# Optimization experiments

Hardware: AMD Instinct MI355X
Metric: run time of the kernel (lower is better)

The kernel has to match this reference:

```python
import jax, jax.numpy as jnp
import numpy as np

K = 32        # number of negative samples
MARGIN = 1.0  # ranking margin
N_NODES = 8192
D_FEAT = 128
N_ANCHOR = 512
CHUNK = 128   # anchor chunk for cdist to bound the [chunk,N,d] intermediate


def l1_cdist(X, Y):
    # X: [A, d], Y: [N, d] -> [A, N]; chunk over A so the abs-diff tensor
    # is [CHUNK, N, d] (~0.5GB here) instead of [A, N, d].
    A, d = X.shape
    def f(xc):  # xc: [CHUNK, d]
        return jnp.sum(jnp.abs(xc[:, None, :] - Y[None, :, :]), axis=-1)
    out = jax.lax.map(f, X.reshape(-1, CHUNK, d))  # [A/CHUNK, CHUNK, N]
    return out.reshape(A, Y.shape[0])


def l1_rowdist(a, b):
    # a, b: [..., d] -> [...]: per-row L1 distance
    return jnp.sum(jnp.abs(a - b), axis=-1)


def setup_inputs() -> dict:
    key = jax.random.key(0)
    k1, k2, k3, k4 = jax.random.split(key, 4)
    out1 = jax.random.normal(k1, (N_NODES, D_FEAT), dtype=jnp.float32)
    out2 = jax.random.normal(k2, (N_NODES, D_FEAT), dtype=jnp.float32)
    anchor1 = jax.random.randint(k3, (N_ANCHOR,), 0, N_NODES, dtype=jnp.int64 if jax.config.jax_enable_x64 else jnp.int32)
    anchor2 = jax.random.randint(k4, (N_ANCHOR,), 0, N_NODES, dtype=jnp.int64 if jax.config.jax_enable_x64 else jnp.int32)
    return {"out1": out1, "out2": out2, "anchor1": anchor1, "anchor2": anchor2}


def reference(out1, out2, anchor1, anchor2):
    a1 = out1[anchor1]  # [A, d]
    a2 = out2[anchor2]  # [A, d]

    # Negative sampling: k NEAREST nodes in the other graph (argsort ascending,
    # take first k). Indices only -> no gradient path (matches numpy detach).
    _, neg1 = jax.lax.top_k(-l1_cdist(a1, out2), K)  # [A, K] into out2
    _, neg2 = jax.lax.top_k(-l1_cdist(a2, out1), K)  # [A, K] into out1

    neg_emb1 = out2[neg1]  # [A, K, d]
    neg_emb2 = out1[neg2]  # [A, K, d]

    D = l1_rowdist(a1, a2) + MARGIN          # [A]
    B1 = -l1_rowdist(a1[:, None, :], neg_emb1)  # [A, K]
    B2 = -l1_rowdist(a2[:, None, :], neg_emb2)  # [A, K]

    L1 = jnp.sum(jax.nn.relu(D[:, None] + B1))
    L2 = jnp.sum(jax.nn.relu(D[:, None] + B2))
    return (L1 + L2) / (anchor1.shape[0] * K)
```

## Files before the change

kernel.cpp:

```cpp
#include <hip/hip_runtime.h>


#define NN 8192
#define DF 128
#define NA 512
#define KK 32
#define CCAP 256


__device__ __forceinline__ float wave_reduce_f(float x) {
#pragma unroll
  for (int off = 32; off > 0; off >>= 1) x += __shfl_down(x, off);
  return x;
}

__device__ __forceinline__ int wave_reduce_i(int x) {
#pragma unroll
  for (int off = 32; off > 0; off >>= 1) x += __shfl_down(x, off);
  return x;
}

__device__ __forceinline__ unsigned umin2(unsigned a, unsigned b) {
  return a < b ? a : b;
}

__device__ __forceinline__ unsigned minpair(unsigned w_) {
  return umin2(w_ & 0xFFFFu, w_ >> 16);
}

__device__ __forceinline__ unsigned sad8(unsigned a, unsigned b,
                                         unsigned acc) {
#if __has_builtin(__builtin_amdgcn_sad_u8)
  return __builtin_amdgcn_sad_u8(a, b, acc);
#else
#pragma unroll
  for (int i = 0; i < 4; ++i) {
    const int av = (int)((a >> (8 * i)) & 0xFFu);
    const int bv = (int)((b >> (8 * i)) & 0xFFu);
    acc += (unsigned)(av > bv ? av - bv : bv - av);
  }
  return acc;
#endif
}

__device__ __forceinline__ unsigned q8(float x) {
  const float f = fmaxf(fmaf(x, 16.0f, 128.5f), 0.0f);
  return umin2((unsigned)f, 255u);
}

__device__ __forceinline__ unsigned q8x4(float4 v) {
  return q8(v.x) | (q8(v.y) << 8) | (q8(v.z) << 16) | (q8(v.w) << 24);
}

__device__ __forceinline__ uint2 quant8u8(float4 a, float4 b) {
  uint2 r;
  r.x = q8x4(a);
  r.y = q8x4(b);
  return r;
}


__global__ __launch_bounds__(256, 2) void dist_kernel(
    const float* __restrict__ out1, const float* __restrict__ out2,
    const int* __restrict__ anchor1, const int* __restrict__ anchor2,
    unsigned short* __restrict__ dist16, float* __restrict__ out) {
  const int tid = threadIdx.x;
  const int nb = blockIdx.x;
  const int ab = blockIdx.y;
  const int dir = blockIdx.z;
  const float* nodes = dir ? out1 : out2;
  const float* asrc = dir ? out2 : out1;
  const int* aidx = dir ? anchor2 : anchor1;
  const int n0 = nb * 128;
  const int a0 = ab * 128;

  if (nb == 0 && ab == 0 && dir == 0 && tid == 0) *out = 0.0f;

  __shared__ union {
    struct {
      unsigned nds[128][34];
      unsigned ads[128][34];
    } t;
    unsigned short stage16[32][136];
  } sm;
  __shared__ int aind[128];

  if (tid < 128) aind[tid] = aidx[a0 + tid];

  unsigned acc[8][8];
#pragma unroll
  for (int i = 0; i < 8; ++i)
#pragma unroll
    for (int j = 0; j < 8; ++j) acc[i][j] = 0u;

  const int tn = tid & 15;
  const int ta = tid >> 4;

  __syncthreads();
#pragma unroll
  for (int r = 0; r < 8; ++r) {
    const int f = tid + 256 * r;
    const int row = f >> 4;
    const int q = f & 15;
    const float* src = nodes + (size_t)(n0 + row) * DF + q * 8;
    const float4 v0 = *(const float4*)(src);
    const float4 v1 = *(const float4*)(src + 4);
    *(uint2*)&sm.t.nds[row][q * 2] = quant8u8(v0, v1);
  }
#pragma unroll
  for (int r = 0; r < 8; ++r) {
    const int f = tid + 256 * r;
    const int row = f >> 4;
    const int q = f & 15;
    const float* src = asrc + (size_t)aind[row] * DF + q * 8;
    const float4 v0 = *(const float4*)(src);
    const float4 v1 = *(const float4*)(src + 4);
    *(uint2*)&sm.t.ads[row][q * 2] = quant8u8(v0, v1);
  }
  __syncthreads();

#pragma unroll 1
  for (int d8 = 0; d8 < 16; ++d8) {
    uint2 nv[8], av[8];
#pragma unroll
    for (int i = 0; i < 8; ++i)
      nv[i] = *(const uint2*)&sm.t.nds[tn + 16 * i][d8 * 2];
#pragma unroll
    for (int j = 0; j < 8; ++j)
      av[j] = *(const uint2*)&sm.t.ads[ta + 16 * j][d8 * 2];
#pragma unroll
    for (int i = 0; i < 8; ++i)
#pragma unroll
      for (int j = 0; j < 8; ++j) {
        const unsigned s = sad8(nv[i].x, av[j].x, acc[i][j]);
        acc[i][j] = sad8(nv[i].y, av[j].y, s);
      }
  }

  const size_t rowbase = (size_t)(dir * NA + a0) * NN + n0;
#pragma unroll
  for (int stg = 0; stg < 4; ++stg) {
    __syncthreads();
#pragma unroll
    for (int jn = 0; jn < 2; ++jn) {
      const int jj = stg * 2 + jn;
#pragma unroll
      for (int i = 0; i < 8; ++i) {
        sm.stage16[ta + 16 * jn][tn + 16 * i] =
            (unsigned short)umin2(acc[i][jj], 65535u);
      }
    }
    __syncthreads();
#pragma unroll
    for (int s = 0; s < 2; ++s) {
      const int f = tid + 256 * s;
      const int r = f >> 4;
      const int c8 = f & 15;
      const uint4 v = *(const uint4*)&sm.stage16[r][c8 * 8];
      *(uint4*)(dist16 + rowbase + (size_t)(stg * 32 + r) * NN + c8 * 8) = v;
    }
  }
}


__global__ __launch_bounds__(256) void select_kernel(
    const unsigned short* __restrict__ dist16, const float* __restrict__ out1,
    const float* __restrict__ out2, const int* __restrict__ anchor1,
    const int* __restrict__ anchor2, float* __restrict__ out) {
  const int tid = threadIdx.x;
  const int lane = tid & 63, w = tid >> 6;
  const int row = blockIdx.x;
  const int a = row & (NA - 1);

  __shared__ unsigned mins[256];
  __shared__ unsigned cand[CCAP];
  __shared__ int cnt;
  __shared__ unsigned Tsh;
  __shared__ float dred[2];
  __shared__ int wcnt[4];
  __shared__ float fred[4];
  __shared__ int cred[4];

  const uint4* drow = (const uint4*)(dist16 + (size_t)row * NN);
  const float inv = 1.0f / 16.0f;

  {
    float p = 0.f;
    if (tid < DF) {
      const int r1 = anchor1[a];
      const int r2 = anchor2[a];
      p = fabsf(out1[(size_t)r1 * DF + tid] - out2[(size_t)r2 * DF + tid]);
    }
    p = wave_reduce_f(p);
    if (tid < DF && lane == 0) dred[w] = p;
  }
  if (tid == 0) cnt = 0;

  uint4 v4[4];
#pragma unroll
  for (int g = 0; g < 4; ++g) v4[g] = drow[tid + 256 * g];

  unsigned m = 0xFFFFFFFFu;
#pragma unroll
  for (int g = 0; g < 4; ++g) {
    m = umin2(m, minpair(v4[g].x));
    m = umin2(m, minpair(v4[g].y));
    m = umin2(m, minpair(v4[g].z));
    m = umin2(m, minpair(v4[g].w));
  }
  mins[tid] = m;
  __syncthreads();

  if (w == 0) {
    const unsigned pm =
        umin2(umin2(mins[lane], mins[lane + 64]),
              umin2(mins[lane + 128], mins[lane + 192]));
    unsigned T = 0;
#pragma unroll 1
    for (int b = 15; b >= 0; --b) {
      const unsigned mid = T | (1u << b);
      if ((int)__popcll(__ballot(pm < mid)) < KK) T = mid;
    }
    if (lane == 0) Tsh = T;
  }
  __syncthreads();
  const unsigned T = Tsh;

#pragma unroll
  for (int g = 0; g < 4; ++g) {
    const unsigned ww[4] = {v4[g].x, v4[g].y, v4[g].z, v4[g].w};
#pragma unroll
    for (int k = 0; k < 4; ++k) {
      const unsigned lo = ww[k] & 0xFFFFu, hi = ww[k] >> 16;
      if (lo <= T) { int q = atomicAdd(&cnt, 1); if (q < CCAP) cand[q] = lo; }
      if (hi <= T) { int q = atomicAdd(&cnt, 1); if (q < CCAP) cand[q] = hi; }
    }
  }
  __syncthreads();
  const int C = cnt;
  const float Dv = dred[0] + dred[1] + 1.0f;

  if (C <= CCAP) {
    if (w != 0) return;
    unsigned v[4];
#pragma unroll
    for (int k = 0; k < 4; ++k)
      v[k] = (lane + 64 * k < C) ? cand[lane + 64 * k] : 0xFFFFFFFFu;

    unsigned P = 0;
#pragma unroll 1
    for (int b = 15; b >= 0; --b) {
      const unsigned mid = P | (1u << b);
      int c = 0;
#pragma unroll
      for (int k = 0; k < 4; ++k) c += (int)__popcll(__ballot(v[k] < mid));
      if (c < KK) P = mid;
    }

    float s = 0.f;
    int c = 0;
#pragma unroll
    for (int k = 0; k < 4; ++k) {
      c += (int)__popcll(__ballot(v[k] < P));
      if (v[k] < P) {
        const float t = Dv - (float)v[k] * inv;
        s += (t > 0.f) ? t : 0.f;
      }
    }
    s = wave_reduce_f(s);
    if (lane == 0) {
      float tt = Dv - (float)P * inv;
      if (tt < 0.f) tt = 0.f;
      atomicAdd(out, (s + (float)(KK - c) * tt) * (1.0f / (float)(NA * KK)));
    }
  } else {
    unsigned P = 0;
#pragma unroll 1
    for (int b = 15; b >= 0; --b) {
      const unsigned mid = P | (1u << b);
      int c = 0;
#pragma unroll
      for (int g = 0; g < 4; ++g) {
        const unsigned ww[4] = {v4[g].x, v4[g].y, v4[g].z, v4[g].w};
#pragma unroll
        for (int k = 0; k < 4; ++k) {
          c += (int)__popcll(__ballot((ww[k] & 0xFFFFu) < mid));
          c += (int)__popcll(__ballot((ww[k] >> 16) < mid));
        }
      }
      if (lane == 0) wcnt[w] = c;
      __syncthreads();
      const int tot = wcnt[0] + wcnt[1] + wcnt[2] + wcnt[3];
      __syncthreads();
      if (tot < KK) P = mid;
    }
    float s = 0.f;
    int c = 0;
#pragma unroll
    for (int g = 0; g < 4; ++g) {
      const unsigned ww[4] = {v4[g].x, v4[g].y, v4[g].z, v4[g].w};
#pragma unroll
      for (int k = 0; k < 4; ++k) {
        const unsigned lo = ww[k] & 0xFFFFu, hi = ww[k] >> 16;
        if (lo < P) {
          const float t = Dv - (float)lo * inv;
          s += (t > 0.f) ? t : 0.f;
          c += 1;
        }
        if (hi < P) {
          const float t = Dv - (float)hi * inv;
          s += (t > 0.f) ? t : 0.f;
          c += 1;
        }
      }
    }
    s = wave_reduce_f(s);
    c = wave_reduce_i(c);
    if (lane == 0) {
      fred[w] = s;
      cred[w] = c;
    }
    __syncthreads();
    if (tid == 0) {
      const float stot = fred[0] + fred[1] + fred[2] + fred[3];
      const int ctot = cred[0] + cred[1] + cred[2] + cred[3];
      float tt = Dv - (float)P * inv;
      if (tt < 0.f) tt = 0.f;
      atomicAdd(out,
                (stot + (float)(KK - ctot) * tt) * (1.0f / (float)(NA * KK)));
    }
  }
}


__device__ __forceinline__ float compute_D_block(
    const float* __restrict__ out1, const float* __restrict__ out2,
    const int* __restrict__ anchor1, const int* __restrict__ anchor2, int a) {
  __shared__ float dred[4];
  const int tid = threadIdx.x;
  float p = 0.f;
  if (tid < DF) {
    const int r1 = anchor1[a];
    const int r2 = anchor2[a];
    p = fabsf(out1[(size_t)r1 * DF + tid] - out2[(size_t)r2 * DF + tid]);
  }
  p = wave_reduce_f(p);
  const int lane = tid & 63, wid = tid >> 6;
  if (lane == 0) dred[wid] = p;
  __syncthreads();
  return dred[0] + dred[1] + dred[2] + dred[3] + 1.0f;
}

__global__ __launch_bounds__(256) void fused_kernel(
    const float* __restrict__ out1, const float* __restrict__ out2,
    const int* __restrict__ anchor1, const int* __restrict__ anchor2,
    float* __restrict__ out) {
  const int tid = threadIdx.x;
  const int row = blockIdx.x;
  const int dir = row >> 9;
  const int a = row & (NA - 1);
  const float* nodes = dir ? out1 : out2;
  const float* asrc = dir ? out2 : out1;
  const int* aidx = dir ? anchor2 : anchor1;

  __shared__ float ars[DF];
  __shared__ int redi[4];
  __shared__ float redf[4];
  if (tid < DF / 4) {
    const int arow = aidx[a];
    *(float4*)&ars[tid * 4] =
        *(const float4*)(asrc + (size_t)arow * DF + tid * 4);
  }
  __syncthreads();

  unsigned u[32];
  for (int i = 0; i < 32; ++i) {
    const int n = tid + 256 * i;
    const float4* nrow = (const float4*)(nodes + (size_t)n * DF);
    float dsum = 0.f;
    for (int d4 = 0; d4 < DF / 4; ++d4) {
      const float4 t = nrow[d4];
      const float4 av = *(const float4*)&ars[d4 * 4];
      dsum += fabsf(t.x - av.x) + fabsf(t.y - av.y) + fabsf(t.z - av.z) +
              fabsf(t.w - av.w);
    }
    u[i] = __float_as_uint(dsum);
  }
  __syncthreads();

  const float Dv = compute_D_block(out1, out2, anchor1, anchor2, a);
  const int lane = tid & 63, wid = tid >> 6;

  unsigned P = 0;
#pragma unroll 1
  for (int b = 30; b >= 0; --b) {
    const unsigned mid = P | (1u << b);
    int c = 0;
#pragma unroll
    for (int i = 0; i < 32; ++i) c += (u[i] < mid) ? 1 : 0;
    c = wave_reduce_i(c);
    __syncthreads();
    if (lane == 0) redi[wid] = c;
    __syncthreads();
    const int tot = redi[0] + redi[1] + redi[2] + redi[3];
    if (tot < KK) P = mid;
  }

  float s = 0.f;
  int c = 0;
#pragma unroll
  for (int i = 0; i < 32; ++i) {
    if (u[i] < P) {
      const float t = Dv - __uint_as_float(u[i]);
      s += (t > 0.f) ? t : 0.f;
      c += 1;
    }
  }
  s = wave_reduce_f(s);
  c = wave_reduce_i(c);
  __syncthreads();
  if (lane == 0) {
    redf[wid] = s;
    redi[wid] = c;
  }
  __syncthreads();
  if (tid == 0) {
    float stot = redf[0] + redf[1] + redf[2] + redf[3];
    const int ctot = redi[0] + redi[1] + redi[2] + redi[3];
    float tt = Dv - __uint_as_float(P);
    if (tt < 0.f) tt = 0.f;
    stot += (float)(KK - ctot) * tt;
    atomicAdd(out, stot * (1.0f / (float)(NA * KK)));
  }
}


extern "C" void kernel_launch(void* const* d_in, const int* in_sizes, int n_in,
                              void* d_out, int out_size, void* d_ws,
                              size_t ws_size, hipStream_t stream) {
  const float* out1 = (const float*)d_in[0];
  const float* out2 = (const float*)d_in[1];
  const int* anchor1 = (const int*)d_in[2];
  const int* anchor2 = (const int*)d_in[3];
  float* out = (float*)d_out;

  const size_t need = (size_t)2 * NA * NN * sizeof(unsigned short);
  if (ws_size >= need) {
    unsigned short* dist16 = (unsigned short*)d_ws;
    dim3 g1(NN / 128, NA / 128, 2);
    dist_kernel<<<g1, 256, 0, stream>>>(out1, out2, anchor1, anchor2, dist16,
                                        out);
    select_kernel<<<2 * NA, 256, 0, stream>>>(dist16, out1, out2, anchor1,
                                              anchor2, out);
  } else {
    (void)hipMemsetAsync(d_out, 0, sizeof(float), stream);
    fused_kernel<<<2 * NA, 256, 0, stream>>>(out1, out2, anchor1, anchor2, out);
  }
}
```

Baseline: 100.3 us.

## Fuse distance and top-k selection into one cooperative kernel with grid syncs

Replaces the two-kernel path (write a full 16-bit distance matrix, then per-row selection) with a single cooperative kernel. Each block keeps its 128x128 tile of distances in registers, publishes per-tile minima, derives a per-row threshold after a grid sync, and emits only candidates under the threshold to a small buffer for a final per-row selection. This removes the 16 MB distance write and re-read and one launch. In exchange it adds three grid-wide barriers, global atomics on candidate counters, and a slow per-row recompute fallback when a row overflows the candidate cap.

Measured after the change: 291.2 us. 2.9x slower.

```diff
diff --git a/kernel.cpp b/kernel.cpp
--- a/kernel.cpp
+++ b/kernel.cpp
@@ -1,4 +1,7 @@
 #include <hip/hip_runtime.h>
+#include <hip/hip_cooperative_groups.h>
+
+namespace cg = cooperative_groups;
 
 
 #define NN 8192
@@ -57,6 +60,280 @@
   r.x = q8x4(a);
   r.y = q8x4(b);
   return r;
+}
+
+
+__global__ __launch_bounds__(256, 2) void coop_kernel(
+    const float* __restrict__ out1, const float* __restrict__ out2,
+    const int* __restrict__ anchor1, const int* __restrict__ anchor2,
+    unsigned short* __restrict__ minbuf,
+    unsigned short* __restrict__ Tbuf,
+    int* __restrict__ cntbuf,
+    unsigned short* __restrict__ candbuf,
+    float* __restrict__ out) {
+  const int tid = threadIdx.x;
+  const int lane = tid & 63, w = tid >> 6;
+  const int bid = blockIdx.x;
+
+  __shared__ union {
+    struct {
+      unsigned nds[128][34];
+      unsigned ads[128][34];
+    } t;
+    struct {
+      unsigned aq[32];
+    } fb;
+  } sm;
+  __shared__ int aind[128];
+  __shared__ unsigned short Tlds[128];
+  __shared__ float dred[2];
+  __shared__ int redi[4];
+  __shared__ float redf[4];
+
+  const int nb = bid & 63;
+  const int ab = (bid >> 6) & 3;
+  const int dir = bid >> 8;
+  const float* nodes = dir ? out1 : out2;
+  const float* asrc = dir ? out2 : out1;
+  const int* aidx = dir ? anchor2 : anchor1;
+  const int n0 = nb * 128;
+  const int a0 = ab * 128;
+
+  if (bid == 0) {
+    if (tid == 0) *out = 0.0f;
+#pragma unroll
+    for (int r = 0; r < 4; ++r) cntbuf[tid + 256 * r] = 0;
+  }
+
+  if (tid < 128) aind[tid] = aidx[a0 + tid];
+
+  unsigned acc[8][8];
+#pragma unroll
+  for (int i = 0; i < 8; ++i)
+#pragma unroll
+    for (int j = 0; j < 8; ++j) acc[i][j] = 0u;
+
+  const int tn = tid & 15;
+  const int ta = tid >> 4;
+
+  __syncthreads();
+#pragma unroll
+  for (int r = 0; r < 8; ++r) {
+    const int f = tid + 256 * r;
+    const int row = f >> 4;
+    const int q = f & 15;
+    const float* src = nodes + (size_t)(n0 + row) * DF + q * 8;
+    const float4 v0 = *(const float4*)(src);
+    const float4 v1 = *(const float4*)(src + 4);
+    *(uint2*)&sm.t.nds[row][q * 2] = quant8u8(v0, v1);
+  }
+#pragma unroll
+  for (int r = 0; r < 8; ++r) {
+    const int f = tid + 256 * r;
+    const int row = f >> 4;
+    const int q = f & 15;
+    const float* src = asrc + (size_t)aind[row] * DF + q * 8;
+    const float4 v0 = *(const float4*)(src);
+    const float4 v1 = *(const float4*)(src + 4);
+    *(uint2*)&sm.t.ads[row][q * 2] = quant8u8(v0, v1);
+  }
+  __syncthreads();
+
+#pragma unroll 1
+  for (int d8 = 0; d8 < 16; ++d8) {
+    uint2 nv[8], av[8];
+#pragma unroll
+    for (int i = 0; i < 8; ++i)
+      nv[i] = *(const uint2*)&sm.t.nds[tn + 16 * i][d8 * 2];
+#pragma unroll
+    for (int j = 0; j < 8; ++j)
+      av[j] = *(const uint2*)&sm.t.ads[ta + 16 * j][d8 * 2];
+#pragma unroll
+    for (int i = 0; i < 8; ++i)
+#pragma unroll
+      for (int j = 0; j < 8; ++j) {
+        const unsigned s = sad8(nv[i].x, av[j].x, acc[i][j]);
+        acc[i][j] = sad8(nv[i].y, av[j].y, s);
+      }
+  }
+
+#pragma unroll
+  for (int j = 0; j < 8; ++j) {
+    unsigned mn = acc[0][j];
+#pragma unroll
+    for (int i = 1; i < 8; ++i) mn = umin2(mn, acc[i][j]);
+#pragma unroll
+    for (int off = 1; off < 16; off <<= 1)
+      mn = umin2(mn, (unsigned)__shfl_xor((int)mn, off));
+    if (tn == 0)
+      minbuf[(size_t)(dir * NA + a0 + ta + 16 * j) * 64 + nb] =
+          (unsigned short)mn;
+  }
+
+  cg::this_grid().sync();
+
+  if (w < 2) {
+    const int row = bid + 512 * w;
+    const unsigned pm = (unsigned)minbuf[(size_t)row * 64 + lane];
+    unsigned T = 0;
+#pragma unroll 1
+    for (int b = 14; b >= 0; --b) {
+      const unsigned mid = T | (1u << b);
+      if ((int)__popcll(__ballot(pm < mid)) < KK) T = mid;
+    }
+    if (lane == 0) Tbuf[row] = (unsigned short)T;
+  }
+
+  cg::this_grid().sync();
+
+  if (tid < 128) Tlds[tid] = Tbuf[dir * NA + a0 + tid];
+  __syncthreads();
+#pragma unroll
+  for (int j = 0; j < 8; ++j) {
+    const int row = dir * NA + a0 + ta + 16 * j;
+    const unsigned Tj = (unsigned)Tlds[ta + 16 * j];
+#pragma unroll
+    for (int i = 0; i < 8; ++i) {
+      if (acc[i][j] <= Tj) {
+        const int pos = atomicAdd(&cntbuf[row], 1);
+        if (pos < CCAP)
+          candbuf[(size_t)row * CCAP + pos] = (unsigned short)acc[i][j];
+      }
+    }
+  }
+
+  cg::this_grid().sync();
+
+  const float inv = 1.0f / 16.0f;
+#pragma unroll 1
+  for (int rr = 0; rr < 2; ++rr) {
+    const int row = bid + 512 * rr;
+    const int a = row & (NA - 1);
+
+    {
+      float p = 0.f;
+      if (tid < DF) {
+        const int r1 = anchor1[a];
+        const int r2 = anchor2[a];
+        p = fabsf(out1[(size_t)r1 * DF + tid] - out2[(size_t)r2 * DF + tid]);
+      }
+      p = wave_reduce_f(p);
+      if (tid < DF && lane == 0) dred[w] = p;
+    }
+    __syncthreads();
+    const float Dv = dred[0] + dred[1] + 1.0f;
+    const int C = cntbuf[row];
+
+    if (C <= CCAP) {
+      if (w == 0) {
+        unsigned v[4];
+#pragma unroll
+        for (int k = 0; k < 4; ++k)
+          v[k] = (lane + 64 * k < C)
+                     ? (unsigned)candbuf[(size_t)row * CCAP + lane + 64 * k]
+                     : 0xFFFFFFFFu;
+
+        unsigned P = 0;
+#pragma unroll 1
+        for (int b = 14; b >= 0; --b) {
+          const unsigned mid = P | (1u << b);
+          int c = 0;
+#pragma unroll
+          for (int k = 0; k < 4; ++k) c += (int)__popcll(__ballot(v[k] < mid));
+          if (c < KK) P = mid;
+        }
+
+        float s = 0.f;
+        int c = 0;
+#pragma unroll
+        for (int k = 0; k < 4; ++k) {
+          c += (int)__popcll(__ballot(v[k] < P));
+          if (v[k] < P) {
+            const float t = Dv - (float)v[k] * inv;
+            s += (t > 0.f) ? t : 0.f;
+          }
+        }
+        s = wave_reduce_f(s);
+        if (lane == 0) {
+          float tt = Dv - (float)P * inv;
+          if (tt < 0.f) tt = 0.f;
+          atomicAdd(out,
+                    (s + (float)(KK - c) * tt) * (1.0f / (float)(NA * KK)));
+        }
+      }
+    } else {
+      const int dir2 = row >> 9;
+      const float* nodes2 = dir2 ? out1 : out2;
+      const float* asrc2 = dir2 ? out2 : out1;
+      const int* aidx2 = dir2 ? anchor2 : anchor1;
+      if (tid < 16) {
+        const int arow = aidx2[a];
+        const float* srcp = asrc2 + (size_t)arow * DF + tid * 8;
+        const float4 f0 = *(const float4*)(srcp);
+        const float4 f1 = *(const float4*)(srcp + 4);
+        const uint2 qq = quant8u8(f0, f1);
+        sm.fb.aq[tid * 2] = qq.x;
+        sm.fb.aq[tid * 2 + 1] = qq.y;
+      }
+      __syncthreads();
+      unsigned u[32];
+#pragma unroll 1
+      for (int i = 0; i < 32; ++i) {
+        const int n = tid + 256 * i;
+        unsigned d = 0;
+#pragma unroll
+        for (int q = 0; q < 16; ++q) {
+          const float* srcp = nodes2 + (size_t)n * DF + q * 8;
+          const float4 f0 = *(const float4*)(srcp);
+          const float4 f1 = *(const float4*)(srcp + 4);
+          const uint2 qq = quant8u8(f0, f1);
+          d = sad8(qq.x, sm.fb.aq[q * 2], d);
+          d = sad8(qq.y, sm.fb.aq[q * 2 + 1], d);
+        }
+        u[i] = d;
+      }
+      unsigned P = 0;
+#pragma unroll 1
+      for (int b = 14; b >= 0; --b) {
+        const unsigned mid = P | (1u << b);
+        int c = 0;
+#pragma unroll
+        for (int i = 0; i < 32; ++i) c += (u[i] < mid) ? 1 : 0;
+        c = wave_reduce_i(c);
+        if (lane == 0) redi[w] = c;
+        __syncthreads();
+        const int tot = redi[0] + redi[1] + redi[2] + redi[3];
+        __syncthreads();
+        if (tot < KK) P = mid;
+      }
+      float s = 0.f;
+      int c = 0;
+#pragma unroll
+      for (int i = 0; i < 32; ++i) {
+        if (u[i] < P) {
+          const float t = Dv - (float)u[i] * inv;
+          s += (t > 0.f) ? t : 0.f;
+          c += 1;
+        }
+      }
+      s = wave_reduce_f(s);
+      c = wave_reduce_i(c);
+      if (lane == 0) {
+        redf[w] = s;
+        redi[w] = c;
+      }
+      __syncthreads();
+      if (tid == 0) {
+        const float stot = redf[0] + redf[1] + redf[2] + redf[3];
+        const int ctot = redi[0] + redi[1] + redi[2] + redi[3];
+        float tt = Dv - (float)P * inv;
+        if (tt < 0.f) tt = 0.f;
+        atomicAdd(out, (stot + (float)(KK - ctot) * tt) *
+                           (1.0f / (float)(NA * KK)));
+      }
+    }
+    __syncthreads();
+  }
 }
 
 
@@ -162,7 +439,6 @@
   }
 }
 
-
 __global__ __launch_bounds__(256) void select_kernel(
     const unsigned short* __restrict__ dist16, const float* __restrict__ out1,
     const float* __restrict__ out2, const int* __restrict__ anchor1,
@@ -212,9 +488,8 @@
   __syncthreads();
 
   if (w == 0) {
-    const unsigned pm =
-        umin2(umin2(mins[lane], mins[lane + 64]),
-              umin2(mins[lane + 128], mins[lane + 192]));
+    const unsigned pm = umin2(umin2(mins[lane], mins[lane + 64]),
+                              umin2(mins[lane + 128], mins[lane + 192]));
     unsigned T = 0;
 #pragma unroll 1
     for (int b = 15; b >= 0; --b) {
@@ -446,6 +721,18 @@
 
   const size_t need = (size_t)2 * NA * NN * sizeof(unsigned short);
   if (ws_size >= need) {
+    unsigned short* minbuf = (unsigned short*)d_ws;
+    unsigned short* Tbuf = (unsigned short*)((char*)d_ws + 131072);
+    int* cntbuf = (int*)((char*)d_ws + 133120);
+    unsigned short* candbuf = (unsigned short*)((char*)d_ws + 137216);
+
+    void* kargs[] = {(void*)&out1,   (void*)&out2,   (void*)&anchor1,
+                     (void*)&anchor2, (void*)&minbuf, (void*)&Tbuf,
+                     (void*)&cntbuf,  (void*)&candbuf, (void*)&out};
+    const hipError_t e = hipLaunchCooperativeKernel(
+        (const void*)coop_kernel, dim3(512), dim3(256), kargs, 0, stream);
+    if (e == hipSuccess) return;
+
     unsigned short* dist16 = (unsigned short*)d_ws;
     dim3 g1(NN / 128, NA / 128, 2);
     dist_kernel<<<g1, 256, 0, stream>>>(out1, out2, anchor1, anchor2, dist16,
```
